# Optimization experiments

Measured on AMD Instinct MI355X. Metric: run time of the kernel, lower is better.

The kernel has to match this reference:

```python
import jax, jax.numpy as jnp
import numpy as np

B = 16384
INPUT_DIM = 2048
HIDDEN = 1536
N_COMP = 256
N_LAYERS = 32
TOP_K = 4


def setup_inputs() -> dict:
    key = jax.random.key(0)
    ks = jax.random.split(key, 12)
    s_in = 1.0 / np.sqrt(INPUT_DIM)
    s_h = 1.0 / np.sqrt(HIDDEN)
    s_3 = 1.0 / np.sqrt(3)
    return {
        "x": jax.random.normal(ks[0], (B, INPUT_DIM), dtype=jnp.float32),
        "layer_idx": 3,
        "embed": jax.random.normal(ks[1], (N_LAYERS, INPUT_DIM), dtype=jnp.float32),
        "enc_w1": jax.random.uniform(ks[2], (INPUT_DIM, HIDDEN), jnp.float32, -s_in, s_in),
        "enc_b1": jax.random.uniform(ks[3], (HIDDEN,), jnp.float32, -s_in, s_in),
        "enc_w2": jax.random.uniform(ks[4], (HIDDEN, N_COMP), jnp.float32, -s_h, s_h),
        "enc_b2": jax.random.uniform(ks[5], (N_COMP,), jnp.float32, -s_h, s_h),
        "components": jax.random.normal(ks[6], (N_COMP, 3), dtype=jnp.float32),
        "dec_w1": jax.random.uniform(ks[7], (3, HIDDEN), jnp.float32, -s_3, s_3),
        "dec_b1": jax.random.uniform(ks[8], (HIDDEN,), jnp.float32, -s_3, s_3),
        "dec_w2": jax.random.uniform(ks[9], (HIDDEN, INPUT_DIM), jnp.float32, -s_h, s_h),
        "dec_b2": jax.random.uniform(ks[10], (INPUT_DIM,), jnp.float32, -s_h, s_h),
    }


def reference(x, layer_idx, embed, enc_w1, enc_b1, enc_w2, enc_b2,
              components, dec_w1, dec_b1, dec_w2, dec_b2):
    # x: (B, D). Add per-layer embedding row.
    x = x + embed[layer_idx]
    # Encoder MLP: Linear -> GELU (exact, erf-based like torch default) -> Linear
    h = jax.nn.gelu(x @ enc_w1 + enc_b1, approximate=False)
    logits = h @ enc_w2 + enc_b2                     # (B, C)
    # Top-k gated masked softmax: softmax over only the top_k logits per row.
    vals, idx = jax.lax.top_k(logits, TOP_K)         # (B, K), (B, K)
    w = jax.nn.softmax(vals, axis=-1)                # (B, K)
    # Sparse mix: equivalent to masked_fill(-inf) softmax @ components
    pts = jnp.einsum('bk,bkc->bc', w, components[idx])  # (B, 3)
    # Decoder MLP
    d = jax.nn.gelu(pts @ dec_w1 + dec_b1, approximate=False)
    decoded = d @ dec_w2 + dec_b2                    # (B, D)
    encoded = jnp.broadcast_to(components[None], (x.shape[0], N_COMP, 3))
    return encoded, decoded
```

## Files before the change

kernel.cpp:

```cpp
#include <hip/hip_runtime.h>


typedef float  f32x4  __attribute__((ext_vector_type(4)));
typedef short  short8 __attribute__((ext_vector_type(8)));

#define DEVINL __device__ __forceinline__

constexpr int  NB      = 16384;
constexpr int  IN_DIM  = 2048;
constexpr int  HID     = 1536;
constexpr int  NC      = 256;
constexpr long ENC_ELEMS = (long)NB * NC * 3;
constexpr float TAU = 2e-5f;
constexpr int  MAXR = 64;
constexpr int  NKT1 = IN_DIM / 32;
constexpr int  NKT2 = HID / 32;

DEVINL unsigned short f2bf(float f) {
  unsigned int u = __builtin_bit_cast(unsigned int, f);
  u = u + 0x7fffu + ((u >> 16) & 1u);
  return (unsigned short)(u >> 16);
}
DEVINL float bf2f(unsigned short h) {
  unsigned int u = ((unsigned int)h) << 16;
  return __builtin_bit_cast(float, u);
}
DEVINL float gelu_f(float v) {
  return 0.5f * v * (1.0f + erff(v * 0.70710678118654752440f));
}
DEVINL void llds16(const void* g, void* l) {
  __builtin_amdgcn_global_load_lds(
      (const __attribute__((address_space(1))) void*)g,
      (__attribute__((address_space(3))) void*)l, 16, 0, 0);
}
DEVINL f32x4 mfma_bf16(short8 a, short8 b, f32x4 c) {
  return __builtin_amdgcn_mfma_f32_16x16x32_bf16(a, b, c, 0, 0, 0);
}
DEVINL long packed_off(long tileIdx, int rowp, int kq, int e) {
  int slot = kq ^ ((rowp >> 1) & 3);
  return (tileIdx * 512 + rowp * 4 + slot) * 8 + e;
}

__global__ __launch_bounds__(256) void transpose_split_kernel(
    const float* __restrict__ in, int K, int N, int nkt,
    unsigned short* __restrict__ outH, unsigned short* __restrict__ outL)
{
  __shared__ float t[32][33];
  int tx = threadIdx.x & 31, ty = threadIdx.x >> 5;
  int n0 = blockIdx.x * 32, k0 = blockIdx.y * 32;
#pragma unroll
  for (int i = 0; i < 4; ++i)
    t[ty + i * 8][tx] = in[(long)(k0 + ty + i * 8) * N + n0 + tx];
  __syncthreads();

  int n = n0 + tx;
  int ntile = n >> 7, rowp = n & 127;
  int Kt = k0 >> 5;
  int j = ty & 3;
  long off = packed_off((long)ntile * nkt + Kt, rowp, j, 0);
  if (ty < 4) {
    short8 hv;
#pragma unroll
    for (int e = 0; e < 8; ++e) hv[e] = (short)f2bf(t[j * 8 + e][tx]);
    *(short8*)(outH + off) = hv;
  } else if (outL) {
    short8 lv;
#pragma unroll
    for (int e = 0; e < 8; ++e) {
      float f = t[j * 8 + e][tx];
      lv[e] = (short)f2bf(f - bf2f(f2bf(f)));
    }
    *(short8*)(outL + off) = lv;
  }
}

__global__ __launch_bounds__(256) void split_x_kernel(
    const float* __restrict__ x, const float* __restrict__ embedMat,
    const int* __restrict__ liPtr,
    unsigned short* __restrict__ Xh, unsigned short* __restrict__ Xl)
{
  long g = (long)blockIdx.x * 256 + threadIdx.x;
  int  li = liPtr[0];
  int  Mtile = (int)(g >> 15);
  int  rem = (int)(g & 32767);
  int  Kt = rem >> 9;
  int  b  = rem & 511;
  int  rowp = b >> 2, slot = b & 3;
  int  kq = slot ^ ((rowp >> 1) & 3);
  long grow = (long)Mtile * 128 + rowp;
  int  k = Kt * 32 + kq * 8;
  const float* xr = x + grow * IN_DIM + k;
  const float* er = embedMat + (long)li * IN_DIM + k;
  f32x4 a0 = *(const f32x4*)(xr);
  f32x4 a1 = *(const f32x4*)(xr + 4);
  f32x4 e0 = *(const f32x4*)(er);
  f32x4 e1 = *(const f32x4*)(er + 4);
  short8 hv, lv;
#pragma unroll
  for (int j2 = 0; j2 < 4; ++j2) {
    float f = a0[j2] + e0[j2];
    unsigned short hb = f2bf(f);
    hv[j2] = (short)hb; lv[j2] = (short)f2bf(f - bf2f(hb));
  }
#pragma unroll
  for (int j2 = 0; j2 < 4; ++j2) {
    float f = a1[j2] + e1[j2];
    unsigned short hb = f2bf(f);
    hv[4 + j2] = (short)hb; lv[4 + j2] = (short)f2bf(f - bf2f(hb));
  }
  *(short8*)(Xh + g * 8) = hv;
  *(short8*)(Xl + g * 8) = lv;
}

template<bool SPLIT, int OUT_MODE, bool GELU>
__global__ __launch_bounds__(256) void gemm2_kernel(
    const unsigned short* __restrict__ Ah, const unsigned short* __restrict__ Al,
    const unsigned short* __restrict__ Bh, const unsigned short* __restrict__ Bl,
    int nkt, const float* __restrict__ bias, float* __restrict__ Cf,
    unsigned short* __restrict__ Ch, unsigned short* __restrict__ Cl,
    long ldc, int nktOut, int nbn)
{
  __shared__ alignas(16) unsigned short sAh[4096];
  __shared__ alignas(16) unsigned short sAl[SPLIT ? 4096 : 8];
  __shared__ alignas(16) unsigned short sBh[4096];
  __shared__ alignas(16) unsigned short sBl[SPLIT ? 4096 : 8];
  __shared__ float sBias[128];

  int tid = threadIdx.x;
  int nwg = gridDim.x, q = nwg >> 3, b0 = blockIdx.x;
  int sw = (b0 & 7) * q + (b0 >> 3);
  int bm = sw / nbn, bn = sw % nbn;

  if (tid < 128) sBias[tid] = bias[bn * 128 + tid];

  int wid = tid >> 6, lane = tid & 63;
  int wm = wid >> 1, wn = wid & 1;
  int l15 = lane & 15, kq = lane >> 4;

  f32x4 acc[4][4] = {};

  for (int kt = 0; kt < nkt; ++kt) {
    __syncthreads();
    {
      const char* gA = (const char*)Ah + ((long)(bm * nkt + kt)) * 8192 + tid * 16;
      llds16(gA,        (char*)sAh + tid * 16);
      llds16(gA + 4096, (char*)sAh + 4096 + tid * 16);
    }
    if constexpr (SPLIT) {
      const char* gA = (const char*)Al + ((long)(bm * nkt + kt)) * 8192 + tid * 16;
      llds16(gA,        (char*)sAl + tid * 16);
      llds16(gA + 4096, (char*)sAl + 4096 + tid * 16);
    }
    {
      const char* gB = (const char*)Bh + ((long)(bn * nkt + kt)) * 8192 + tid * 16;
      llds16(gB,        (char*)sBh + tid * 16);
      llds16(gB + 4096, (char*)sBh + 4096 + tid * 16);
    }
    if constexpr (SPLIT) {
      const char* gB = (const char*)Bl + ((long)(bn * nkt + kt)) * 8192 + tid * 16;
      llds16(gB,        (char*)sBl + tid * 16);
      llds16(gB + 4096, (char*)sBl + 4096 + tid * 16);
    }
    __syncthreads();

    short8 bh[4], bl[4];
#pragma unroll
    for (int n = 0; n < 4; ++n) {
      int rowp = wn * 64 + n * 16 + l15;
      int idx = (rowp * 4 + (kq ^ ((rowp >> 1) & 3))) * 8;
      bh[n] = *(const short8*)&sBh[idx];
      if constexpr (SPLIT) bl[n] = *(const short8*)&sBl[idx];
    }
#pragma unroll
    for (int m = 0; m < 4; ++m) {
      int rowp = wm * 64 + m * 16 + l15;
      int idx = (rowp * 4 + (kq ^ ((rowp >> 1) & 3))) * 8;
      short8 ah = *(const short8*)&sAh[idx];
      short8 al;
      if constexpr (SPLIT) al = *(const short8*)&sAl[idx];
#pragma unroll
      for (int n = 0; n < 4; ++n) {
        acc[m][n] = mfma_bf16(ah, bh[n], acc[m][n]);
        if constexpr (SPLIT) {
          acc[m][n] = mfma_bf16(al, bh[n], acc[m][n]);
          acc[m][n] = mfma_bf16(ah, bl[n], acc[m][n]);
        }
      }
    }
  }

#pragma unroll
  for (int m = 0; m < 4; ++m) {
#pragma unroll
    for (int n = 0; n < 4; ++n) {
      int  gcol = bn * 128 + wn * 64 + n * 16 + l15;
      float bb  = sBias[wn * 64 + n * 16 + l15];
#pragma unroll
      for (int r = 0; r < 4; ++r) {
        long grow = (long)bm * 128 + wm * 64 + m * 16 + kq * 4 + r;
        float v = acc[m][n][r] + bb;
        if constexpr (GELU) v = gelu_f(v);
        if constexpr (OUT_MODE == 0) {
          Cf[grow * ldc + gcol] = v;
        } else {
          int Mt = (int)(grow >> 7), rowpo = (int)(grow & 127);
          int Kt = gcol >> 5, kqo = (gcol >> 3) & 3, e = gcol & 7;
          long off = packed_off((long)Mt * nktOut + Kt, rowpo, kqo, e);
          unsigned short hb = f2bf(v);
          Ch[off] = hb;
          Cl[off] = f2bf(v - bf2f(hb));
        }
      }
    }
  }
}

__global__ __launch_bounds__(256) void topk_kernel(
    const float* __restrict__ logits, const float* __restrict__ comp,
    float* __restrict__ pts, int* __restrict__ rescueCnt, int* __restrict__ rescueList)
{
  int wid = threadIdx.x >> 6, lane = threadIdx.x & 63;
  long row = (long)blockIdx.x * 4 + wid;
  f32x4 v4 = *(const f32x4*)(logits + row * NC + lane * 4);
  float a[4] = {v4[0], v4[1], v4[2], v4[3]};

  float tv[5]; int ti[5];
#pragma unroll
  for (int t = 0; t < 5; ++t) {
    float lv = a[0]; int li = lane * 4;
#pragma unroll
    for (int i = 1; i < 4; ++i)
      if (a[i] > lv) { lv = a[i]; li = lane * 4 + i; }
#pragma unroll
    for (int off = 32; off >= 1; off >>= 1) {
      float ov = __shfl_xor(lv, off);
      int   oi = __shfl_xor(li, off);
      if (ov > lv || (ov == lv && oi < li)) { lv = ov; li = oi; }
    }
    tv[t] = lv; ti[t] = li;
    if (t < 4 && (li >> 2) == lane) a[li & 3] = -INFINITY;
  }

  float m = tv[0], w[4], s = 0.f;
#pragma unroll
  for (int t = 0; t < 4; ++t) { w[t] = expf(tv[t] - m); s += w[t]; }
  float inv = 1.0f / s;
  if (lane < 3) {
    float p = 0.f;
#pragma unroll
    for (int t = 0; t < 4; ++t) p += w[t] * inv * comp[ti[t] * 3 + lane];
    pts[row * 3 + lane] = p;
  }
  if (lane == 0 && (tv[3] - tv[4]) < TAU) {
    int pos = atomicAdd(rescueCnt, 1);
    rescueList[pos] = (int)row;
  }
}

__global__ __launch_bounds__(256) void rescue_h1_kernel(
    const float* __restrict__ x, const float* __restrict__ embedMat,
    const int* __restrict__ liPtr, const float* __restrict__ W1,
    const int* __restrict__ cnt, const int* __restrict__ list,
    double* __restrict__ partial)
{
  int b = blockIdx.x;
  int s = b / 24, rem = b % 24;
  int cc = rem >> 2, kp = rem & 3;
  int n = *cnt;
  if (s >= n || s >= MAXR) return;
  int row = list[s];
  __shared__ double xd[512];
  int tid = threadIdx.x;
  int li = liPtr[0];
  int k0 = kp * 512;
  for (int j = tid; j < 512; j += 256)
    xd[j] = (double)x[(long)row * IN_DIM + k0 + j]
          + (double)embedMat[(long)li * IN_DIM + k0 + j];
  __syncthreads();
  int c = cc * 256 + tid;
  const float* wp = W1 + (long)k0 * HID + c;
  double s0 = 0, s1 = 0, s2 = 0, s3 = 0;
  for (int k = 0; k < 512; k += 4) {
    s0 += xd[k]     * (double)wp[(long)k * HID];
    s1 += xd[k + 1] * (double)wp[(long)(k + 1) * HID];
    s2 += xd[k + 2] * (double)wp[(long)(k + 2) * HID];
    s3 += xd[k + 3] * (double)wp[(long)(k + 3) * HID];
  }
  partial[((long)(s * 6 + cc) * 4 + kp) * 256 + tid] = (s0 + s1) + (s2 + s3);
}

__global__ __launch_bounds__(256) void rescue_h2_kernel(
    const float* __restrict__ b1, const int* __restrict__ cnt,
    const double* __restrict__ partial, double* __restrict__ hbuf)
{
  int b = blockIdx.x;
  int s = b / 6, cc = b % 6;
  int n = *cnt;
  if (s >= n || s >= MAXR) return;
  int tid = threadIdx.x;
  long base = ((long)(s * 6 + cc) * 4) * 256 + tid;
  double v = (double)b1[cc * 256 + tid]
           + ((partial[base] + partial[base + 256])
            + (partial[base + 512] + partial[base + 768]));
  hbuf[(long)s * HID + cc * 256 + tid]
      = 0.5 * v * (1.0 + erf(v * 0.70710678118654752440));
}

__global__ __launch_bounds__(256) void rescue_logits_kernel(
    const float* __restrict__ W2, const float* __restrict__ b2,
    const float* __restrict__ comp, const int* __restrict__ cnt,
    const int* __restrict__ list, const double* __restrict__ hbuf,
    float* __restrict__ pts)
{
  int s = blockIdx.x;
  int n = *cnt;
  if (s >= n || s >= MAXR) return;
  __shared__ double hd[HID];
  __shared__ double ld[NC];
  int tid = threadIdx.x;
  for (int j = tid; j < HID; j += 256) hd[j] = hbuf[(long)s * HID + j];
  __syncthreads();
  {
    const float* wp = W2 + tid;
    double a0 = 0, a1 = 0, a2 = 0, a3 = 0;
    for (int k = 0; k < HID; k += 4) {
      a0 += hd[k]     * (double)wp[(long)k * NC];
      a1 += hd[k + 1] * (double)wp[(long)(k + 1) * NC];
      a2 += hd[k + 2] * (double)wp[(long)(k + 2) * NC];
      a3 += hd[k + 3] * (double)wp[(long)(k + 3) * NC];
    }
    ld[tid] = (double)b2[tid] + ((a0 + a1) + (a2 + a3));
  }
  __syncthreads();
  if (tid == 0) {
    int row = list[s];
    int idx[4]; double val[4];
    unsigned long long mask[4] = {0, 0, 0, 0};
    for (int t = 0; t < 4; ++t) {
      double bv = -1e300; int bi = 0;
      for (int j = 0; j < NC; ++j) {
        if ((mask[j >> 6] >> (j & 63)) & 1ull) continue;
        if (ld[j] > bv) { bv = ld[j]; bi = j; }
      }
      idx[t] = bi; val[t] = bv; mask[bi >> 6] |= 1ull << (bi & 63);
    }
    double m = val[0], w[4], sum = 0;
    for (int t = 0; t < 4; ++t) { w[t] = exp(val[t] - m); sum += w[t]; }
    for (int c = 0; c < 3; ++c) {
      double p = 0;
      for (int t = 0; t < 4; ++t) p += (w[t] / sum) * (double)comp[idx[t] * 3 + c];
      pts[(long)row * 3 + c] = (float)p;
    }
  }
}

__global__ __launch_bounds__(256) void rescue_slow_kernel(
    const float* __restrict__ x, const float* __restrict__ embedMat,
    const int* __restrict__ liPtr, const float* __restrict__ W1,
    const float* __restrict__ b1, const float* __restrict__ W2,
    const float* __restrict__ b2, const float* __restrict__ comp,
    float* __restrict__ pts, const int* __restrict__ cnt, const int* __restrict__ list)
{
  __shared__ double xd[IN_DIM];
  __shared__ double hd[HID];
  __shared__ double ld[NC];
  int tid = threadIdx.x;
  int li = liPtr[0];
  int n = *cnt;
  for (int it = MAXR + blockIdx.x; it < n; it += gridDim.x) {
    int row = list[it];
    const float* xr = x + (long)row * IN_DIM;
    const float* er = embedMat + (long)li * IN_DIM;
    for (int j = tid; j < IN_DIM; j += 256)
      xd[j] = (double)xr[j] + (double)er[j];
    __syncthreads();
    for (int c = tid; c < HID; c += 256) {
      double s0 = 0, s1 = 0, s2 = 0, s3 = 0;
      const float* wp = W1 + c;
      for (int k = 0; k < IN_DIM; k += 4) {
        s0 += xd[k]     * (double)wp[(long)k * HID];
        s1 += xd[k + 1] * (double)wp[(long)(k + 1) * HID];
        s2 += xd[k + 2] * (double)wp[(long)(k + 2) * HID];
        s3 += xd[k + 3] * (double)wp[(long)(k + 3) * HID];
      }
      double s = (double)b1[c] + ((s0 + s1) + (s2 + s3));
      hd[c] = 0.5 * s * (1.0 + erf(s * 0.70710678118654752440));
    }
    __syncthreads();
    {
      int c = tid;
      double s0 = 0, s1 = 0, s2 = 0, s3 = 0;
      const float* wp = W2 + c;
      for (int k = 0; k < HID; k += 4) {
        s0 += hd[k]     * (double)wp[(long)k * NC];
        s1 += hd[k + 1] * (double)wp[(long)(k + 1) * NC];
        s2 += hd[k + 2] * (double)wp[(long)(k + 2) * NC];
        s3 += hd[k + 3] * (double)wp[(long)(k + 3) * NC];
      }
      ld[c] = (double)b2[c] + ((s0 + s1) + (s2 + s3));
    }
    __syncthreads();
    if (tid == 0) {
      int idx[4]; double val[4];
      unsigned long long mask[4] = {0, 0, 0, 0};
      for (int t = 0; t < 4; ++t) {
        double bv = -1e300; int bi = 0;
        for (int j = 0; j < NC; ++j) {
          if ((mask[j >> 6] >> (j & 63)) & 1ull) continue;
          if (ld[j] > bv) { bv = ld[j]; bi = j; }
        }
        idx[t] = bi; val[t] = bv; mask[bi >> 6] |= 1ull << (bi & 63);
      }
      double m = val[0], w[4], s = 0;
      for (int t = 0; t < 4; ++t) { w[t] = exp(val[t] - m); s += w[t]; }
      for (int c = 0; c < 3; ++c) {
        double p = 0;
        for (int t = 0; t < 4; ++t) p += (w[t] / s) * (double)comp[idx[t] * 3 + c];
        pts[(long)row * 3 + c] = (float)p;
      }
    }
    __syncthreads();
  }
}

__global__ __launch_bounds__(256) void dec_a_kernel(
    const float* __restrict__ pts, const float* __restrict__ W1d,
    const float* __restrict__ b1d, unsigned short* __restrict__ dout)
{
  int  j = (blockIdx.x % 6) * 256 + threadIdx.x;
  long b = blockIdx.x / 6;
  const float* p = pts + b * 3;
  float s = fmaf(p[0], W1d[j], fmaf(p[1], W1d[HID + j], fmaf(p[2], W1d[2 * HID + j], b1d[j])));
  int Mt = (int)(b >> 7), rowp = (int)(b & 127);
  int Kt = j >> 5, kq = (j >> 3) & 3, e = j & 7;
  dout[packed_off((long)Mt * NKT2 + Kt, rowp, kq, e)] = f2bf(gelu_f(s));
}

__global__ __launch_bounds__(256) void enc_out_kernel(
    const float* __restrict__ comp, float* __restrict__ out)
{
  long base = (long)blockIdx.x * 768;
  int  t = threadIdx.x;
  out[base + t]       = comp[t];
  out[base + 256 + t] = comp[256 + t];
  out[base + 512 + t] = comp[512 + t];
}

__global__ void zero_cnt_kernel(int* c) { if (threadIdx.x == 0) *c = 0; }

extern "C" void kernel_launch(void* const* d_in, const int* in_sizes, int n_in,
                              void* d_out, int out_size, void* d_ws, size_t ws_size,
                              hipStream_t stream) {
  const float* x     = (const float*)d_in[0];
  const int*   liPtr = (const int*)  d_in[1];
  const float* embed = (const float*)d_in[2];
  const float* W1    = (const float*)d_in[3];
  const float* b1    = (const float*)d_in[4];
  const float* W2    = (const float*)d_in[5];
  const float* b2    = (const float*)d_in[6];
  const float* comp  = (const float*)d_in[7];
  const float* W1d   = (const float*)d_in[8];
  const float* b1d   = (const float*)d_in[9];
  const float* W2d   = (const float*)d_in[10];
  const float* b2d   = (const float*)d_in[11];
  float* out = (float*)d_out;

  char* w = (char*)d_ws;
  unsigned short* W1hT = (unsigned short*)(w);
  unsigned short* W1lT = (unsigned short*)(w + 6291456);
  unsigned short* W2hT = (unsigned short*)(w + 12582912);
  unsigned short* W2lT = (unsigned short*)(w + 13369344);
  unsigned short* W2dT = (unsigned short*)(w + 14155776);
  constexpr size_t A0 = 20447232;

  unsigned short* Xh = (unsigned short*)(w + A0);
  unsigned short* Xl = (unsigned short*)(w + A0 + 67108864);
  unsigned short* Hh = (unsigned short*)(w + A0 + 134217728);
  unsigned short* Hl = (unsigned short*)(w + A0 + 184549376);
  float*  logits  = (float*)(w + A0);
  float*  pts     = (float*)(w + A0 + 16777216);
  int*    cnt     = (int*)  (w + A0 + 16973824);
  int*    list    = (int*)  (w + A0 + 16974080);
  double* partial = (double*)(w + A0 + 17108992);
  double* hbuf    = (double*)(w + A0 + 20254720);
  unsigned short* dbuf = Xl;

  transpose_split_kernel<<<dim3(HID / 32, IN_DIM / 32), 256, 0, stream>>>(W1, IN_DIM, HID, NKT1, W1hT, W1lT);
  transpose_split_kernel<<<dim3(NC / 32, HID / 32),     256, 0, stream>>>(W2, HID, NC, NKT2, W2hT, W2lT);
  transpose_split_kernel<<<dim3(IN_DIM / 32, HID / 32), 256, 0, stream>>>(W2d, HID, IN_DIM, NKT2, W2dT, nullptr);

  split_x_kernel<<<NB * IN_DIM / 2048, 256, 0, stream>>>(x, embed, liPtr, Xh, Xl);

  gemm2_kernel<true, 2, true><<<(NB / 128) * (HID / 128), 256, 0, stream>>>(
      Xh, Xl, W1hT, W1lT, NKT1, b1, nullptr, Hh, Hl, 0, NKT2, HID / 128);
  gemm2_kernel<true, 0, false><<<(NB / 128) * (NC / 128), 256, 0, stream>>>(
      Hh, Hl, W2hT, W2lT, NKT2, b2, logits, nullptr, nullptr, NC, 0, NC / 128);

  zero_cnt_kernel<<<1, 64, 0, stream>>>(cnt);
  topk_kernel<<<NB / 4, 256, 0, stream>>>(logits, comp, pts, cnt, list);
  rescue_h1_kernel<<<MAXR * 24, 256, 0, stream>>>(x, embed, liPtr, W1, cnt, list, partial);
  rescue_h2_kernel<<<MAXR * 6,  256, 0, stream>>>(b1, cnt, partial, hbuf);
  rescue_logits_kernel<<<MAXR,  256, 0, stream>>>(W2, b2, comp, cnt, list, hbuf, pts);
  rescue_slow_kernel<<<64, 256, 0, stream>>>(x, embed, liPtr, W1, b1, W2, b2, comp, pts, cnt, list);

  dec_a_kernel<<<NB * (HID / 256), 256, 0, stream>>>(pts, W1d, b1d, dbuf);
  gemm2_kernel<false, 0, false><<<(NB / 128) * (IN_DIM / 128), 256, 0, stream>>>(
      dbuf, nullptr, W2dT, nullptr, NKT2, b2d, out + ENC_ELEMS, nullptr, nullptr,
      IN_DIM, 0, IN_DIM / 128);

  enc_out_kernel<<<NB, 256, 0, stream>>>(comp, out);
}
```

Baseline: 799.6 us.

## Add double-buffered 512-thread pipelined GEMMs for encoder layer1 and decoder output

Adds two new GEMM kernels with 128x256 output tiles and 8 waves per block, used for the first encoder GEMM (split-bf16 with GELU epilogue) and the decoder output GEMM. Each kernel double-buffers its LDS tiles and issues the next k-tile's global-to-LDS loads in stages interleaved with the MFMA phases. It uses explicit barriers, waitcnt, sched_barrier and setprio to overlap memory with compute and to cut B-tile reloads per output. The trade-offs are higher LDS and register use with one block per CU, plus many more barriers per k-step.

```diff
diff --git a/kernel.cpp b/kernel.cpp
--- a/kernel.cpp
+++ b/kernel.cpp
@@ -39,6 +39,9 @@
 DEVINL long packed_off(long tileIdx, int rowp, int kq, int e) {
   int slot = kq ^ ((rowp >> 1) & 3);
   return (tileIdx * 512 + rowp * 4 + slot) * 8 + e;
+}
+DEVINL int swz_idx(int rowp, int kq) {
+  return (rowp * 4 + (kq ^ ((rowp >> 1) & 3))) * 8;
 }
 
 __global__ __launch_bounds__(256) void transpose_split_kernel(
@@ -112,6 +115,277 @@
   *(short8*)(Xl + g * 8) = lv;
 }
 
+__global__ __launch_bounds__(512, 1) void gemm_pipe_split_kernel(
+    const unsigned short* __restrict__ Ah, const unsigned short* __restrict__ Al,
+    const unsigned short* __restrict__ Bh, const unsigned short* __restrict__ Bl,
+    int nkt, const float* __restrict__ bias,
+    unsigned short* __restrict__ Ch, unsigned short* __restrict__ Cl,
+    int nktOut, int nbn)
+{
+  __shared__ alignas(16) unsigned short sAh[2][4096];
+  __shared__ alignas(16) unsigned short sAl[2][4096];
+  __shared__ alignas(16) unsigned short sBh[2][8192];
+  __shared__ alignas(16) unsigned short sBl[2][8192];
+  __shared__ float sBias[256];
+
+  int tid = threadIdx.x;
+  int nwg = gridDim.x, q = nwg >> 3, b0 = blockIdx.x;
+  int sw = (b0 & 7) * q + (b0 >> 3);
+  int bm = sw / nbn, bn = sw % nbn;
+
+  if (tid < 256) sBias[tid] = bias[bn * 256 + tid];
+
+  int wid = tid >> 6, lane = tid & 63;
+  int wm = wid >> 2, wn = wid & 3;
+  int l15 = lane & 15, kq = lane >> 4;
+
+  int aidx[4], bidx[4];
+#pragma unroll
+  for (int m = 0; m < 4; ++m) aidx[m] = swz_idx(wm * 64 + m * 16 + l15, kq);
+#pragma unroll
+  for (int n = 0; n < 4; ++n) {
+    int r = wn * 64 + n * 16 + l15;
+    bidx[n] = (r >> 7) * 4096 + swz_idx(r & 127, kq);
+  }
+
+  f32x4 acc[4][4] = {};
+
+  {
+    long at = (long)(bm * nkt);
+    llds16((const char*)Ah + at * 8192 + tid * 16, (char*)sAh[0] + tid * 16);
+    llds16((const char*)Al + at * 8192 + tid * 16, (char*)sAl[0] + tid * 16);
+    long bt0 = (long)((bn * 2) * nkt), bt1 = (long)((bn * 2 + 1) * nkt);
+    llds16((const char*)Bh + bt0 * 8192 + tid * 16, (char*)sBh[0] + tid * 16);
+    llds16((const char*)Bh + bt1 * 8192 + tid * 16, (char*)sBh[0] + 8192 + tid * 16);
+    llds16((const char*)Bl + bt0 * 8192 + tid * 16, (char*)sBl[0] + tid * 16);
+    llds16((const char*)Bl + bt1 * 8192 + tid * 16, (char*)sBl[0] + 8192 + tid * 16);
+  }
+  asm volatile("s_waitcnt vmcnt(0)");
+  __builtin_amdgcn_sched_barrier(0);
+  __builtin_amdgcn_s_barrier();
+
+  for (int t = 0; t < nkt; ++t) {
+    int cur = t & 1, nxt = cur ^ 1;
+    bool pre = (t + 1 < nkt);
+    short8 ah[4], al[4], bh, bl;
+
+#pragma unroll
+    for (int m = 0; m < 4; ++m) {
+      ah[m] = *(const short8*)&sAh[cur][aidx[m]];
+      al[m] = *(const short8*)&sAl[cur][aidx[m]];
+    }
+    bh = *(const short8*)&sBh[cur][bidx[0]];
+    bl = *(const short8*)&sBl[cur][bidx[0]];
+    if (pre) {
+      long at = (long)(bm * nkt + t + 1);
+      llds16((const char*)Ah + at * 8192 + tid * 16, (char*)sAh[nxt] + tid * 16);
+      llds16((const char*)Al + at * 8192 + tid * 16, (char*)sAl[nxt] + tid * 16);
+    }
+    __builtin_amdgcn_s_barrier();
+    asm volatile("s_waitcnt lgkmcnt(0)");
+    __builtin_amdgcn_sched_barrier(0);
+    __builtin_amdgcn_s_setprio(1);
+#pragma unroll
+    for (int m = 0; m < 4; ++m) {
+      acc[m][0] = mfma_bf16(ah[m], bh, acc[m][0]);
+      acc[m][0] = mfma_bf16(al[m], bh, acc[m][0]);
+      acc[m][0] = mfma_bf16(ah[m], bl, acc[m][0]);
+    }
+    __builtin_amdgcn_s_setprio(0);
+    __builtin_amdgcn_sched_barrier(0);
+    __builtin_amdgcn_s_barrier();
+
+#pragma unroll
+    for (int ph = 1; ph < 4; ++ph) {
+      bh = *(const short8*)&sBh[cur][bidx[ph]];
+      bl = *(const short8*)&sBl[cur][bidx[ph]];
+      if (pre && ph == 1) {
+        long bt0 = (long)((bn * 2) * nkt + t + 1), bt1 = (long)((bn * 2 + 1) * nkt + t + 1);
+        llds16((const char*)Bh + bt0 * 8192 + tid * 16, (char*)sBh[nxt] + tid * 16);
+        llds16((const char*)Bh + bt1 * 8192 + tid * 16, (char*)sBh[nxt] + 8192 + tid * 16);
+      }
+      if (pre && ph == 2) {
+        long bt0 = (long)((bn * 2) * nkt + t + 1), bt1 = (long)((bn * 2 + 1) * nkt + t + 1);
+        llds16((const char*)Bl + bt0 * 8192 + tid * 16, (char*)sBl[nxt] + tid * 16);
+        llds16((const char*)Bl + bt1 * 8192 + tid * 16, (char*)sBl[nxt] + 8192 + tid * 16);
+      }
+      __builtin_amdgcn_s_barrier();
+      asm volatile("s_waitcnt lgkmcnt(0)");
+      __builtin_amdgcn_sched_barrier(0);
+      __builtin_amdgcn_s_setprio(1);
+#pragma unroll
+      for (int m = 0; m < 4; ++m) {
+        acc[m][ph] = mfma_bf16(ah[m], bh, acc[m][ph]);
+        acc[m][ph] = mfma_bf16(al[m], bh, acc[m][ph]);
+        acc[m][ph] = mfma_bf16(ah[m], bl, acc[m][ph]);
+      }
+      __builtin_amdgcn_s_setprio(0);
+      __builtin_amdgcn_sched_barrier(0);
+      __builtin_amdgcn_s_barrier();
+    }
+
+    asm volatile("s_waitcnt vmcnt(0)");
+    __builtin_amdgcn_sched_barrier(0);
+    __builtin_amdgcn_s_barrier();
+  }
+
+#pragma unroll
+  for (int m = 0; m < 4; ++m) {
+#pragma unroll
+    for (int n = 0; n < 4; ++n) {
+      int  gcol = bn * 256 + wn * 64 + n * 16 + l15;
+      float bb  = sBias[wn * 64 + n * 16 + l15];
+#pragma unroll
+      for (int r = 0; r < 4; ++r) {
+        long grow = (long)bm * 128 + wm * 64 + m * 16 + kq * 4 + r;
+        float v = gelu_f(acc[m][n][r] + bb);
+        int Mt = (int)(grow >> 7), rowpo = (int)(grow & 127);
+        int Kt = gcol >> 5, kqo = (gcol >> 3) & 3, e = gcol & 7;
+        long off = packed_off((long)Mt * nktOut + Kt, rowpo, kqo, e);
+        unsigned short hb = f2bf(v);
+        Ch[off] = hb;
+        Cl[off] = f2bf(v - bf2f(hb));
+      }
+    }
+  }
+}
+
+__global__ __launch_bounds__(512, 1) void gemm_pipe_plain_kernel(
+    const unsigned short* __restrict__ Ah, const unsigned short* __restrict__ Bh,
+    int nkt , const float* __restrict__ bias,
+    float* __restrict__ Cf, long ldc, int nbn)
+{
+  __shared__ alignas(16) unsigned short sA[2][8192];
+  __shared__ alignas(16) unsigned short sB[2][16384];
+  __shared__ float sBias[256];
+
+  int tid = threadIdx.x;
+  int nwg = gridDim.x, q = nwg >> 3, b0 = blockIdx.x;
+  int sw = (b0 & 7) * q + (b0 >> 3);
+  int bm = sw / nbn, bn = sw % nbn;
+
+  if (tid < 256) sBias[tid] = bias[bn * 256 + tid];
+
+  int wid = tid >> 6, lane = tid & 63;
+  int wm = wid >> 2, wn = wid & 3;
+  int l15 = lane & 15, kq = lane >> 4;
+
+  int aidx[4], bidx[4];
+#pragma unroll
+  for (int m = 0; m < 4; ++m) aidx[m] = swz_idx(wm * 64 + m * 16 + l15, kq);
+#pragma unroll
+  for (int n = 0; n < 4; ++n) {
+    int r = wn * 64 + n * 16 + l15;
+    bidx[n] = (r >> 7) * 8192 + swz_idx(r & 127, kq);
+  }
+
+  f32x4 acc[4][4] = {};
+  int nks = nkt >> 1;
+
+  {
+#pragma unroll
+    for (int s = 0; s < 2; ++s) {
+      long at = (long)(bm * nkt + s);
+      llds16((const char*)Ah + at * 8192 + tid * 16, (char*)sA[0] + s * 8192 + tid * 16);
+#pragma unroll
+      for (int h = 0; h < 2; ++h) {
+        long bt = (long)((bn * 2 + h) * nkt + s);
+        llds16((const char*)Bh + bt * 8192 + tid * 16,
+               (char*)sB[0] + (h * 2 + s) * 8192 + tid * 16);
+      }
+    }
+  }
+  asm volatile("s_waitcnt vmcnt(0)");
+  __builtin_amdgcn_sched_barrier(0);
+  __builtin_amdgcn_s_barrier();
+
+  for (int t = 0; t < nks; ++t) {
+    int cur = t & 1, nxt = cur ^ 1;
+    bool pre = (t + 1 < nks);
+    short8 ah[4][2], bf[4][2];
+
+#pragma unroll
+    for (int m = 0; m < 4; ++m)
+#pragma unroll
+      for (int s = 0; s < 2; ++s)
+        ah[m][s] = *(const short8*)&sA[cur][s * 4096 + aidx[m]];
+#pragma unroll
+    for (int n = 0; n < 2; ++n)
+#pragma unroll
+      for (int s = 0; s < 2; ++s)
+        bf[n][s] = *(const short8*)&sB[cur][n >= 2 ? 0 : bidx[n] + s * 4096];
+    if (pre) {
+#pragma unroll
+      for (int s = 0; s < 2; ++s) {
+        long at = (long)(bm * nkt + 2 * (t + 1) + s);
+        llds16((const char*)Ah + at * 8192 + tid * 16, (char*)sA[nxt] + s * 8192 + tid * 16);
+      }
+      {
+        long bt0 = (long)((bn * 2) * nkt + 2 * (t + 1));
+        llds16((const char*)Bh + bt0 * 8192 + tid * 16, (char*)sB[nxt] + tid * 16);
+        llds16((const char*)Bh + (bt0 + 1) * 8192 + tid * 16, (char*)sB[nxt] + 4096 * 2 + tid * 16);
+      }
+    }
+    __builtin_amdgcn_s_barrier();
+    asm volatile("s_waitcnt lgkmcnt(0)");
+    __builtin_amdgcn_sched_barrier(0);
+    __builtin_amdgcn_s_setprio(1);
+#pragma unroll
+    for (int n = 0; n < 2; ++n)
+#pragma unroll
+      for (int m = 0; m < 4; ++m)
+#pragma unroll
+        for (int s = 0; s < 2; ++s)
+          acc[m][n] = mfma_bf16(ah[m][s], bf[n][s], acc[m][n]);
+    __builtin_amdgcn_s_setprio(0);
+    __builtin_amdgcn_sched_barrier(0);
+    __builtin_amdgcn_s_barrier();
+
+#pragma unroll
+    for (int n = 2; n < 4; ++n)
+#pragma unroll
+      for (int s = 0; s < 2; ++s)
+        bf[n][s] = *(const short8*)&sB[cur][bidx[n] + s * 4096];
+    if (pre) {
+      long bt1 = (long)((bn * 2 + 1) * nkt + 2 * (t + 1));
+      llds16((const char*)Bh + bt1 * 8192 + tid * 16, (char*)sB[nxt] + 2 * 8192 + tid * 16);
+      llds16((const char*)Bh + (bt1 + 1) * 8192 + tid * 16, (char*)sB[nxt] + 3 * 8192 + tid * 16);
+    }
+    __builtin_amdgcn_s_barrier();
+    asm volatile("s_waitcnt lgkmcnt(0)");
+    __builtin_amdgcn_sched_barrier(0);
+    __builtin_amdgcn_s_setprio(1);
+#pragma unroll
+    for (int n = 2; n < 4; ++n)
+#pragma unroll
+      for (int m = 0; m < 4; ++m)
+#pragma unroll
+        for (int s = 0; s < 2; ++s)
+          acc[m][n] = mfma_bf16(ah[m][s], bf[n][s], acc[m][n]);
+    __builtin_amdgcn_s_setprio(0);
+    __builtin_amdgcn_sched_barrier(0);
+    __builtin_amdgcn_s_barrier();
+
+    asm volatile("s_waitcnt vmcnt(0)");
+    __builtin_amdgcn_sched_barrier(0);
+    __builtin_amdgcn_s_barrier();
+  }
+
+#pragma unroll
+  for (int m = 0; m < 4; ++m) {
+#pragma unroll
+    for (int n = 0; n < 4; ++n) {
+      int  gcol = bn * 256 + wn * 64 + n * 16 + l15;
+      float bb  = sBias[wn * 64 + n * 16 + l15];
+#pragma unroll
+      for (int r = 0; r < 4; ++r) {
+        long grow = (long)bm * 128 + wm * 64 + m * 16 + kq * 4 + r;
+        Cf[grow * ldc + gcol] = acc[m][n][r] + bb;
+      }
+    }
+  }
+}
+
 template<bool SPLIT, int OUT_MODE, bool GELU>
 __global__ __launch_bounds__(256) void gemm2_kernel(
     const unsigned short* __restrict__ Ah, const unsigned short* __restrict__ Al,
@@ -166,15 +440,13 @@
     short8 bh[4], bl[4];
 #pragma unroll
     for (int n = 0; n < 4; ++n) {
-      int rowp = wn * 64 + n * 16 + l15;
-      int idx = (rowp * 4 + (kq ^ ((rowp >> 1) & 3))) * 8;
+      int idx = swz_idx(wn * 64 + n * 16 + l15, kq);
       bh[n] = *(const short8*)&sBh[idx];
       if constexpr (SPLIT) bl[n] = *(const short8*)&sBl[idx];
     }
 #pragma unroll
     for (int m = 0; m < 4; ++m) {
-      int rowp = wm * 64 + m * 16 + l15;
-      int idx = (rowp * 4 + (kq ^ ((rowp >> 1) & 3))) * 8;
+      int idx = swz_idx(wm * 64 + m * 16 + l15, kq);
       short8 ah = *(const short8*)&sAh[idx];
       short8 al;
       if constexpr (SPLIT) al = *(const short8*)&sAl[idx];
@@ -491,8 +763,8 @@
 
   split_x_kernel<<<NB * IN_DIM / 2048, 256, 0, stream>>>(x, embed, liPtr, Xh, Xl);
 
-  gemm2_kernel<true, 2, true><<<(NB / 128) * (HID / 128), 256, 0, stream>>>(
-      Xh, Xl, W1hT, W1lT, NKT1, b1, nullptr, Hh, Hl, 0, NKT2, HID / 128);
+  gemm_pipe_split_kernel<<<(NB / 128) * (HID / 256), 512, 0, stream>>>(
+      Xh, Xl, W1hT, W1lT, NKT1, b1, Hh, Hl, NKT2, HID / 256);
   gemm2_kernel<true, 0, false><<<(NB / 128) * (NC / 128), 256, 0, stream>>>(
       Hh, Hl, W2hT, W2lT, NKT2, b2, logits, nullptr, nullptr, NC, 0, NC / 128);
 
@@ -504,9 +776,8 @@
   rescue_slow_kernel<<<64, 256, 0, stream>>>(x, embed, liPtr, W1, b1, W2, b2, comp, pts, cnt, list);
 
   dec_a_kernel<<<NB * (HID / 256), 256, 0, stream>>>(pts, W1d, b1d, dbuf);
-  gemm2_kernel<false, 0, false><<<(NB / 128) * (IN_DIM / 128), 256, 0, stream>>>(
-      dbuf, nullptr, W2dT, nullptr, NKT2, b2d, out + ENC_ELEMS, nullptr, nullptr,
-      IN_DIM, 0, IN_DIM / 128);
+  gemm_pipe_plain_kernel<<<(NB / 128) * (IN_DIM / 256), 512, 0, stream>>>(
+      dbuf, W2dT, NKT2, b2d, out + ENC_ELEMS, IN_DIM, IN_DIM / 256);
 
   enc_out_kernel<<<NB, 256, 0, stream>>>(comp, out);
 }
```

Result: slower. 820.5 us (+2.6%).

## Replace GEMM kernels with triple-buffered 128x256 tile pipelined kernels

Applied to the files above, without the earlier changes.

Replaces the single-buffered 128x128 GEMM with 512-thread kernels that compute 128x256 output tiles and triple-buffer LDS. Global-to-LDS prefetch of tile t+2 is interleaved with MFMA phases, using explicit vmcnt/lgkmcnt waits, barriers and setprio. The goal is to hide load latency and raise reuse of the A tile. In exchange it uses much more LDS (one block per CU) and depends on a fragile hand-tuned waitcnt schedule.

```diff
diff --git a/kernel.cpp b/kernel.cpp
--- a/kernel.cpp
+++ b/kernel.cpp
@@ -39,6 +39,9 @@
 DEVINL long packed_off(long tileIdx, int rowp, int kq, int e) {
   int slot = kq ^ ((rowp >> 1) & 3);
   return (tileIdx * 512 + rowp * 4 + slot) * 8 + e;
+}
+DEVINL int swz_idx(int rowp, int kq) {
+  return (rowp * 4 + (kq ^ ((rowp >> 1) & 3))) * 8;
 }
 
 __global__ __launch_bounds__(256) void transpose_split_kernel(
@@ -112,88 +115,121 @@
   *(short8*)(Xl + g * 8) = lv;
 }
 
-template<bool SPLIT, int OUT_MODE, bool GELU>
-__global__ __launch_bounds__(256) void gemm2_kernel(
-    const unsigned short* __restrict__ Ah, const unsigned short* __restrict__ Al,
-    const unsigned short* __restrict__ Bh, const unsigned short* __restrict__ Bl,
-    int nkt, const float* __restrict__ bias, float* __restrict__ Cf,
-    unsigned short* __restrict__ Ch, unsigned short* __restrict__ Cl,
-    long ldc, int nktOut, int nbn)
-{
-  __shared__ alignas(16) unsigned short sAh[4096];
-  __shared__ alignas(16) unsigned short sAl[SPLIT ? 4096 : 8];
-  __shared__ alignas(16) unsigned short sBh[4096];
-  __shared__ alignas(16) unsigned short sBl[SPLIT ? 4096 : 8];
-  __shared__ float sBias[128];
+template<int OUT_MODE, bool GELU>
+__global__ __launch_bounds__(512, 1) void pipe_split_kernel(
+    const unsigned short* __restrict__ Ahg, const unsigned short* __restrict__ Alg,
+    const unsigned short* __restrict__ Bhg, const unsigned short* __restrict__ Blg,
+    int nkt, const float* __restrict__ bias,
+    float* __restrict__ Cf, unsigned short* __restrict__ Ch,
+    unsigned short* __restrict__ Cl, long ldc, int nktOut, int nbn)
+{
+  __shared__ alignas(16) unsigned short sAh[3][4096];
+  __shared__ alignas(16) unsigned short sAl[3][4096];
+  __shared__ alignas(16) unsigned short sBh[3][8192];
+  __shared__ alignas(16) unsigned short sBl[3][8192];
+  __shared__ float sBias[256];
 
   int tid = threadIdx.x;
   int nwg = gridDim.x, q = nwg >> 3, b0 = blockIdx.x;
   int sw = (b0 & 7) * q + (b0 >> 3);
   int bm = sw / nbn, bn = sw % nbn;
 
-  if (tid < 128) sBias[tid] = bias[bn * 128 + tid];
+  if (tid < 256) sBias[tid] = bias[bn * 256 + tid];
 
   int wid = tid >> 6, lane = tid & 63;
-  int wm = wid >> 1, wn = wid & 1;
+  int wm = wid >> 2, wn = wid & 3;
   int l15 = lane & 15, kq = lane >> 4;
 
+  int aidx[4], bidx[4];
+#pragma unroll
+  for (int m = 0; m < 4; ++m) aidx[m] = swz_idx(wm * 64 + m * 16 + l15, kq);
+#pragma unroll
+  for (int n = 0; n < 4; ++n) {
+    int r = wn * 64 + n * 16 + l15;
+    bidx[n] = (r >> 7) * 4096 + swz_idx(r & 127, kq);
+  }
+
+  auto stageA = [&](int t, int r) {
+    long at = (long)(bm * nkt + t) * 8192;
+    llds16((const char*)Ahg + at + tid * 16, (char*)sAh[r] + tid * 16);
+    llds16((const char*)Alg + at + tid * 16, (char*)sAl[r] + tid * 16);
+  };
+  auto stageBh = [&](int t, int r) {
+    long t0 = (long)((bn * 2) * nkt + t) * 8192;
+    long t1 = (long)((bn * 2 + 1) * nkt + t) * 8192;
+    llds16((const char*)Bhg + t0 + tid * 16, (char*)sBh[r] + tid * 16);
+    llds16((const char*)Bhg + t1 + tid * 16, (char*)sBh[r] + 8192 + tid * 16);
+  };
+  auto stageBl = [&](int t, int r) {
+    long t0 = (long)((bn * 2) * nkt + t) * 8192;
+    long t1 = (long)((bn * 2 + 1) * nkt + t) * 8192;
+    llds16((const char*)Blg + t0 + tid * 16, (char*)sBl[r] + tid * 16);
+    llds16((const char*)Blg + t1 + tid * 16, (char*)sBl[r] + 8192 + tid * 16);
+  };
+
   f32x4 acc[4][4] = {};
 
-  for (int kt = 0; kt < nkt; ++kt) {
-    __syncthreads();
-    {
-      const char* gA = (const char*)Ah + ((long)(bm * nkt + kt)) * 8192 + tid * 16;
-      llds16(gA,        (char*)sAh + tid * 16);
-      llds16(gA + 4096, (char*)sAh + 4096 + tid * 16);
-    }
-    if constexpr (SPLIT) {
-      const char* gA = (const char*)Al + ((long)(bm * nkt + kt)) * 8192 + tid * 16;
-      llds16(gA,        (char*)sAl + tid * 16);
-      llds16(gA + 4096, (char*)sAl + 4096 + tid * 16);
-    }
-    {
-      const char* gB = (const char*)Bh + ((long)(bn * nkt + kt)) * 8192 + tid * 16;
-      llds16(gB,        (char*)sBh + tid * 16);
-      llds16(gB + 4096, (char*)sBh + 4096 + tid * 16);
-    }
-    if constexpr (SPLIT) {
-      const char* gB = (const char*)Bl + ((long)(bn * nkt + kt)) * 8192 + tid * 16;
-      llds16(gB,        (char*)sBl + tid * 16);
-      llds16(gB + 4096, (char*)sBl + 4096 + tid * 16);
-    }
-    __syncthreads();
-
-    short8 bh[4], bl[4];
+  stageA(0, 0); stageBh(0, 0); stageBl(0, 0);
+  stageA(1, 1); stageBh(1, 1); stageBl(1, 1);
+
+  for (int t = 0; t < nkt; ++t) {
+    int r = t % 3, r2 = (t + 2) % 3;
+    bool pre = (t + 2 < nkt);
+    if (t + 1 < nkt) asm volatile("s_waitcnt vmcnt(6)" ::: "memory");
+    else             asm volatile("s_waitcnt vmcnt(0)" ::: "memory");
+    __builtin_amdgcn_sched_barrier(0);
+    __builtin_amdgcn_s_barrier();
+
+    short8 ah[4], al[4], bh, bl;
+#pragma unroll
+    for (int m = 0; m < 4; ++m) {
+      ah[m] = *(const short8*)&sAh[r][aidx[m]];
+      al[m] = *(const short8*)&sAl[r][aidx[m]];
+    }
+    bh = *(const short8*)&sBh[r][bidx[0]];
+    bl = *(const short8*)&sBl[r][bidx[0]];
+    if (pre) stageA(t + 2, r2);
+    __builtin_amdgcn_s_barrier();
+    asm volatile("s_waitcnt lgkmcnt(0)" ::: "memory");
+    __builtin_amdgcn_sched_barrier(0);
+    __builtin_amdgcn_s_setprio(1);
+#pragma unroll
+    for (int m = 0; m < 4; ++m) {
+      acc[m][0] = mfma_bf16(ah[m], bh, acc[m][0]);
+      acc[m][0] = mfma_bf16(al[m], bh, acc[m][0]);
+      acc[m][0] = mfma_bf16(ah[m], bl, acc[m][0]);
+    }
+    __builtin_amdgcn_s_setprio(0);
+    __builtin_amdgcn_sched_barrier(0);
+    __builtin_amdgcn_s_barrier();
+
+#pragma unroll
+    for (int ph = 1; ph < 4; ++ph) {
+      bh = *(const short8*)&sBh[r][bidx[ph]];
+      bl = *(const short8*)&sBl[r][bidx[ph]];
+      if (pre && ph == 1) stageBh(t + 2, r2);
+      if (pre && ph == 2) stageBl(t + 2, r2);
+      __builtin_amdgcn_s_barrier();
+      asm volatile("s_waitcnt lgkmcnt(0)" ::: "memory");
+      __builtin_amdgcn_sched_barrier(0);
+      __builtin_amdgcn_s_setprio(1);
+#pragma unroll
+      for (int m = 0; m < 4; ++m) {
+        acc[m][ph] = mfma_bf16(ah[m], bh, acc[m][ph]);
+        acc[m][ph] = mfma_bf16(al[m], bh, acc[m][ph]);
+        acc[m][ph] = mfma_bf16(ah[m], bl, acc[m][ph]);
+      }
+      __builtin_amdgcn_s_setprio(0);
+      __builtin_amdgcn_sched_barrier(0);
+      __builtin_amdgcn_s_barrier();
+    }
+  }
+
+#pragma unroll
+  for (int m = 0; m < 4; ++m) {
 #pragma unroll
     for (int n = 0; n < 4; ++n) {
-      int rowp = wn * 64 + n * 16 + l15;
-      int idx = (rowp * 4 + (kq ^ ((rowp >> 1) & 3))) * 8;
-      bh[n] = *(const short8*)&sBh[idx];
-      if constexpr (SPLIT) bl[n] = *(const short8*)&sBl[idx];
-    }
-#pragma unroll
-    for (int m = 0; m < 4; ++m) {
-      int rowp = wm * 64 + m * 16 + l15;
-      int idx = (rowp * 4 + (kq ^ ((rowp >> 1) & 3))) * 8;
-      short8 ah = *(const short8*)&sAh[idx];
-      short8 al;
-      if constexpr (SPLIT) al = *(const short8*)&sAl[idx];
-#pragma unroll
-      for (int n = 0; n < 4; ++n) {
-        acc[m][n] = mfma_bf16(ah, bh[n], acc[m][n]);
-        if constexpr (SPLIT) {
-          acc[m][n] = mfma_bf16(al, bh[n], acc[m][n]);
-          acc[m][n] = mfma_bf16(ah, bl[n], acc[m][n]);
-        }
-      }
-    }
-  }
-
-#pragma unroll
-  for (int m = 0; m < 4; ++m) {
-#pragma unroll
-    for (int n = 0; n < 4; ++n) {
-      int  gcol = bn * 128 + wn * 64 + n * 16 + l15;
+      int  gcol = bn * 256 + wn * 64 + n * 16 + l15;
       float bb  = sBias[wn * 64 + n * 16 + l15];
 #pragma unroll
       for (int r = 0; r < 4; ++r) {
@@ -210,6 +246,130 @@
           Ch[off] = hb;
           Cl[off] = f2bf(v - bf2f(hb));
         }
+      }
+    }
+  }
+}
+
+__global__ __launch_bounds__(512, 1) void pipe_plain_kernel(
+    const unsigned short* __restrict__ Ahg, const unsigned short* __restrict__ Bhg,
+    int nkt , const float* __restrict__ bias,
+    float* __restrict__ Cf, long ldc, int nbn)
+{
+  __shared__ alignas(16) unsigned short sA[3][8192];
+  __shared__ alignas(16) unsigned short sB[3][16384];
+  __shared__ float sBias[256];
+
+  int tid = threadIdx.x;
+  int nwg = gridDim.x, q = nwg >> 3, b0 = blockIdx.x;
+  int sw = (b0 & 7) * q + (b0 >> 3);
+  int bm = sw / nbn, bn = sw % nbn;
+
+  if (tid < 256) sBias[tid] = bias[bn * 256 + tid];
+
+  int wid = tid >> 6, lane = tid & 63;
+  int wm = wid >> 2, wn = wid & 3;
+  int l15 = lane & 15, kq = lane >> 4;
+
+  int aidx[4], bidx[4];
+#pragma unroll
+  for (int m = 0; m < 4; ++m) aidx[m] = swz_idx(wm * 64 + m * 16 + l15, kq);
+#pragma unroll
+  for (int n = 0; n < 4; ++n) {
+    int r = wn * 64 + n * 16 + l15;
+    bidx[n] = (r >> 7) * 8192 + swz_idx(r & 127, kq);
+  }
+
+  int nks = nkt >> 1;
+
+  auto stageA = [&](int t, int r) {
+#pragma unroll
+    for (int s = 0; s < 2; ++s) {
+      long at = (long)(bm * nkt + 2 * t + s) * 8192;
+      llds16((const char*)Ahg + at + tid * 16, (char*)sA[r] + s * 8192 + tid * 16);
+    }
+  };
+  auto stageB = [&](int t, int r, int h) {
+#pragma unroll
+    for (int s = 0; s < 2; ++s) {
+      long bt = (long)((bn * 2 + h) * nkt + 2 * t + s) * 8192;
+      llds16((const char*)Bhg + bt + tid * 16,
+             (char*)sB[r] + (h * 2 + s) * 8192 + tid * 16);
+    }
+  };
+
+  f32x4 acc[4][4] = {};
+
+  stageA(0, 0); stageB(0, 0, 0); stageB(0, 0, 1);
+  stageA(1, 1); stageB(1, 1, 0); stageB(1, 1, 1);
+
+  for (int t = 0; t < nks; ++t) {
+    int r = t % 3, r2 = (t + 2) % 3;
+    bool pre = (t + 2 < nks);
+    if (t + 1 < nks) asm volatile("s_waitcnt vmcnt(6)" ::: "memory");
+    else             asm volatile("s_waitcnt vmcnt(0)" ::: "memory");
+    __builtin_amdgcn_sched_barrier(0);
+    __builtin_amdgcn_s_barrier();
+
+    short8 ah[4][2], bf0[2][2], bf1[2][2];
+#pragma unroll
+    for (int m = 0; m < 4; ++m)
+#pragma unroll
+      for (int s = 0; s < 2; ++s)
+        ah[m][s] = *(const short8*)&sA[r][s * 4096 + aidx[m]];
+#pragma unroll
+    for (int n = 0; n < 2; ++n)
+#pragma unroll
+      for (int s = 0; s < 2; ++s)
+        bf0[n][s] = *(const short8*)&sB[r][bidx[n] + s * 4096];
+    if (pre) { stageA(t + 2, r2); stageB(t + 2, r2, 0); }
+    __builtin_amdgcn_s_barrier();
+    asm volatile("s_waitcnt lgkmcnt(0)" ::: "memory");
+    __builtin_amdgcn_sched_barrier(0);
+    __builtin_amdgcn_s_setprio(1);
+#pragma unroll
+    for (int n = 0; n < 2; ++n)
+#pragma unroll
+      for (int m = 0; m < 4; ++m)
+#pragma unroll
+        for (int s = 0; s < 2; ++s)
+          acc[m][n] = mfma_bf16(ah[m][s], bf0[n][s], acc[m][n]);
+    __builtin_amdgcn_s_setprio(0);
+    __builtin_amdgcn_sched_barrier(0);
+    __builtin_amdgcn_s_barrier();
+
+#pragma unroll
+    for (int n = 0; n < 2; ++n)
+#pragma unroll
+      for (int s = 0; s < 2; ++s)
+        bf1[n][s] = *(const short8*)&sB[r][bidx[n + 2] + s * 4096];
+    if (pre) stageB(t + 2, r2, 1);
+    __builtin_amdgcn_s_barrier();
+    asm volatile("s_waitcnt lgkmcnt(0)" ::: "memory");
+    __builtin_amdgcn_sched_barrier(0);
+    __builtin_amdgcn_s_setprio(1);
+#pragma unroll
+    for (int n = 0; n < 2; ++n)
+#pragma unroll
+      for (int m = 0; m < 4; ++m)
+#pragma unroll
+        for (int s = 0; s < 2; ++s)
+          acc[m][n + 2] = mfma_bf16(ah[m][s], bf1[n][s], acc[m][n + 2]);
+    __builtin_amdgcn_s_setprio(0);
+    __builtin_amdgcn_sched_barrier(0);
+    __builtin_amdgcn_s_barrier();
+  }
+
+#pragma unroll
+  for (int m = 0; m < 4; ++m) {
+#pragma unroll
+    for (int n = 0; n < 4; ++n) {
+      int  gcol = bn * 256 + wn * 64 + n * 16 + l15;
+      float bb  = sBias[wn * 64 + n * 16 + l15];
+#pragma unroll
+      for (int r = 0; r < 4; ++r) {
+        long grow = (long)bm * 128 + wm * 64 + m * 16 + kq * 4 + r;
+        Cf[grow * ldc + gcol] = acc[m][n][r] + bb;
       }
     }
   }
@@ -491,10 +651,10 @@
 
   split_x_kernel<<<NB * IN_DIM / 2048, 256, 0, stream>>>(x, embed, liPtr, Xh, Xl);
 
-  gemm2_kernel<true, 2, true><<<(NB / 128) * (HID / 128), 256, 0, stream>>>(
-      Xh, Xl, W1hT, W1lT, NKT1, b1, nullptr, Hh, Hl, 0, NKT2, HID / 128);
-  gemm2_kernel<true, 0, false><<<(NB / 128) * (NC / 128), 256, 0, stream>>>(
-      Hh, Hl, W2hT, W2lT, NKT2, b2, logits, nullptr, nullptr, NC, 0, NC / 128);
+  pipe_split_kernel<2, true><<<(NB / 128) * (HID / 256), 512, 0, stream>>>(
+      Xh, Xl, W1hT, W1lT, NKT1, b1, nullptr, Hh, Hl, 0, NKT2, HID / 256);
+  pipe_split_kernel<0, false><<<(NB / 128) * (NC / 256), 512, 0, stream>>>(
+      Hh, Hl, W2hT, W2lT, NKT2, b2, logits, nullptr, nullptr, NC, 0, NC / 256);
 
   zero_cnt_kernel<<<1, 64, 0, stream>>>(cnt);
   topk_kernel<<<NB / 4, 256, 0, stream>>>(logits, comp, pts, cnt, list);
@@ -504,9 +664,8 @@
   rescue_slow_kernel<<<64, 256, 0, stream>>>(x, embed, liPtr, W1, b1, W2, b2, comp, pts, cnt, list);
 
   dec_a_kernel<<<NB * (HID / 256), 256, 0, stream>>>(pts, W1d, b1d, dbuf);
-  gemm2_kernel<false, 0, false><<<(NB / 128) * (IN_DIM / 128), 256, 0, stream>>>(
-      dbuf, nullptr, W2dT, nullptr, NKT2, b2d, out + ENC_ELEMS, nullptr, nullptr,
-      IN_DIM, 0, IN_DIM / 128);
+  pipe_plain_kernel<<<(NB / 128) * (IN_DIM / 256), 512, 0, stream>>>(
+      dbuf, W2dT, NKT2, b2d, out + ENC_ELEMS, IN_DIM, IN_DIM / 256);
 
   enc_out_kernel<<<NB, 256, 0, stream>>>(comp, out);
 }
```

After: 847.8 us. +6.0%, slower.
